# Kernel tuning notes

Hardware: AMD Instinct MI355X
Metric: run time of the kernel (lower is better)

The kernel has to match this reference:

```python
import jax, jax.numpy as jnp
import numpy as np

B, S, D = 2, 2048, 1024
H = 16
HD = D // H
MINUS_INFINITY = -1000000000.0


def setup_inputs() -> dict:
    key = jax.random.key(0)
    ks = jax.random.split(key, 6)
    sc = 0.02
    return {
        "x": jax.random.normal(ks[0], (B, S, D), dtype=jnp.float32),
        "Wq": jax.random.normal(ks[1], (D, D), dtype=jnp.float32) * sc,
        "Wk": jax.random.normal(ks[2], (D, D), dtype=jnp.float32) * sc,
        "Wv": jax.random.normal(ks[3], (D, D), dtype=jnp.float32) * sc,
        "Wo": jax.random.normal(ks[4], (D, D), dtype=jnp.float32) * sc,
        "bo": jnp.zeros((D,), dtype=jnp.float32),
    }


def reference(x, Wq, Wk, Wv, Wo, bo):
    b, n, _ = x.shape
    # Linear with transpose_b=True: x @ W.T
    q = jnp.einsum('bnd,ed->bne', x, Wq).reshape(b, n, H, HD).transpose(0, 2, 1, 3)
    k = jnp.einsum('bnd,ed->bne', x, Wk).reshape(b, n, H, HD).transpose(0, 2, 1, 3)
    v = jnp.einsum('bnd,ed->bne', x, Wv).reshape(b, n, H, HD).transpose(0, 2, 1, 3)
    scores = jnp.einsum('bhqd,bhkd->bhqk', q, k) * (1.0 / HD ** 0.5)
    mask = jnp.triu(jnp.ones((n, n), dtype=scores.dtype), k=1) * MINUS_INFINITY
    scores = scores + mask[None, None, :, :]
    attn = jax.nn.softmax(scores, axis=-1)  # dropout prob = 0.0
    ctx = jnp.einsum('bhqk,bhkd->bhqd', attn, v)
    ctx = ctx.transpose(0, 2, 1, 3).reshape(b, n, D)
    return jnp.einsum('bnd,ed->bne', ctx, Wo) + bo
```

## Files before the change

kernel.cpp:

```cpp
#include <hip/hip_runtime.h>
#include <hip/hip_bf16.h>

#define B_  2
#define S_  2048
#define D_  1024
#define H_  16
#define HD_ 64

typedef __attribute__((ext_vector_type(8))) short short8;
typedef __attribute__((ext_vector_type(4))) float f32x4;

__device__ __forceinline__ unsigned short f2b(float f) {
    __hip_bfloat16 h = __float2bfloat16(f);
    unsigned short u;
    __builtin_memcpy(&u, &h, 2);
    return u;
}

__device__ __forceinline__ float exp2_raw(float x) {
    float r;
    asm("v_exp_f32 %0, %1" : "=v"(r) : "v"(x));
    return r;
}

__device__ __forceinline__ unsigned int cvt_pk_bf16(float lo, float hi) {
    unsigned int r;
    asm("v_cvt_pk_bf16_f32 %0, %1, %2" : "=v"(r) : "v"(lo), "v"(hi));
    return r;
}

typedef __attribute__((address_space(1))) const unsigned int g_u32;
typedef __attribute__((address_space(3))) unsigned int l_u32;
__device__ __forceinline__ void gload_lds16(const void* g, void* l) {
    __builtin_amdgcn_global_load_lds((g_u32*)g, (l_u32*)l, 16, 0, 0);
}

__global__ __launch_bounds__(256) void convert_kernel(
    const float* __restrict__ x,  const float* __restrict__ Wq,
    const float* __restrict__ Wk, const float* __restrict__ Wv,
    const float* __restrict__ Wo, unsigned short* __restrict__ dst)
{
    const long long i4 = blockIdx.x * 256 + threadIdx.x;
    const long long e  = i4 * 4;
    const long long M1 = 1048576LL;
    const float* src;
    if      (e < 4 * M1) src = x  + e;
    else if (e < 5 * M1) src = Wq + (e - 4 * M1);
    else if (e < 6 * M1) src = Wk + (e - 5 * M1);
    else if (e < 7 * M1) src = Wv + (e - 6 * M1);
    else                 src = Wo + (e - 7 * M1);
    float4 v = *(const float4*)src;
    unsigned long long pk = (unsigned long long)f2b(v.x)
                          | ((unsigned long long)f2b(v.y) << 16)
                          | ((unsigned long long)f2b(v.z) << 32)
                          | ((unsigned long long)f2b(v.w) << 48);
    *(unsigned long long*)&dst[e] = pk;
}

__global__ __launch_bounds__(256) void qkv_proj_kernel(
    const unsigned short* __restrict__ x,
    const unsigned short* __restrict__ Wq,
    const unsigned short* __restrict__ Wk,
    const unsigned short* __restrict__ Wv,
    unsigned short* __restrict__ q_ws,
    unsigned short* __restrict__ k_ws,
    unsigned short* __restrict__ vT_ws)
{
    __shared__ unsigned short a_lds[128 * 64];
    __shared__ unsigned short b_lds[128 * 64];

    const int m0 = blockIdx.x * 128;
    const int n0 = blockIdx.y * 128;
    const int which = blockIdx.z;
    const unsigned short* W = (which == 0) ? Wq : (which == 1) ? Wk : Wv;

    const int tid  = threadIdx.x;
    const int wave = tid >> 6;
    const int lane = tid & 63;
    const int l15  = lane & 15;
    const int quad = lane >> 4;
    const int wm = (wave & 1) * 64;
    const int wn = (wave >> 1) * 64;
    const int xr = (l15 & 7) << 3;

    f32x4 acc[4][4];
    #pragma unroll
    for (int sm = 0; sm < 4; ++sm)
        #pragma unroll
        for (int sn = 0; sn < 4; ++sn)
            #pragma unroll
            for (int r = 0; r < 4; ++r) acc[sm][sn][r] = 0.f;

    for (int kk = 0; kk < D_; kk += 64) {
        #pragma unroll
        for (int p = 0; p < 4; ++p) {
            const int off = (p * 256 + tid) * 16;
            const int r   = off >> 7;
            const int cs  = ((off & 127) >> 1) ^ ((r & 7) << 3);
            gload_lds16(&x[(m0 + r) * D_ + kk + cs], &a_lds[off >> 1]);
            gload_lds16(&W[(n0 + r) * D_ + kk + cs], &b_lds[off >> 1]);
        }
        __syncthreads();
        #pragma unroll
        for (int kc = 0; kc < 2; ++kc) {
            const int cswz = (kc * 32 + quad * 8) ^ xr;
            short8 af[4], bf[4];
            #pragma unroll
            for (int s = 0; s < 4; ++s) {
                af[s] = *(const short8*)&a_lds[(wm + s * 16 + l15) * 64 + cswz];
                bf[s] = *(const short8*)&b_lds[(wn + s * 16 + l15) * 64 + cswz];
            }
            #pragma unroll
            for (int sm = 0; sm < 4; ++sm)
                #pragma unroll
                for (int sn = 0; sn < 4; ++sn)
                    acc[sm][sn] = __builtin_amdgcn_mfma_f32_16x16x32_bf16(
                        af[sm], bf[sn], acc[sm][sn], 0, 0, 0);
        }
        __syncthreads();
    }

    #pragma unroll
    for (int sm = 0; sm < 4; ++sm) {
        #pragma unroll
        for (int sn = 0; sn < 4; ++sn) {
            const int n  = n0 + wn + sn * 16 + l15;
            const int h  = n >> 6;
            const int hd = n & 63;
            const int mbase = m0 + wm + sm * 16 + quad * 4;
            const int b     = mbase >> 11;
            const int sbase = mbase & 2047;
            if (which == 2) {
                unsigned long long pk =
                      (unsigned long long)cvt_pk_bf16(acc[sm][sn][0], acc[sm][sn][1])
                    | ((unsigned long long)cvt_pk_bf16(acc[sm][sn][2], acc[sm][sn][3]) << 32);
                *(unsigned long long*)&vT_ws[((b * H_ + h) * HD_ + hd) * S_ + sbase] = pk;
            } else if (which == 0) {
                #pragma unroll
                for (int r = 0; r < 4; ++r)
                    q_ws[((b * H_ + h) * S_ + (sbase + r)) * HD_ + hd] =
                        f2b(acc[sm][sn][r] * (0.125f * 1.44269504f));
            } else {
                #pragma unroll
                for (int r = 0; r < 4; ++r)
                    k_ws[((b * H_ + h) * S_ + (sbase + r)) * HD_ + hd] =
                        f2b(acc[sm][sn][r]);
            }
        }
    }
}

__global__ __launch_bounds__(256) void attn_kernel(
    const unsigned short* __restrict__ q_ws,
    const unsigned short* __restrict__ k_ws,
    const unsigned short* __restrict__ vT_ws,
    unsigned short* __restrict__ ctx_ws)
{
    __shared__ unsigned short k_lds[2 * 64 * 64];
    __shared__ unsigned short vT_lds[2 * 64 * 64];

    const int bh = blockIdx.x;
    const int qt = 31 - (int)blockIdx.y;

    const int tid  = threadIdx.x;
    const int wave = tid >> 6;
    const int lane = tid & 63;
    const int l15  = lane & 15;
    const int quad = lane >> 4;
    const int r0   = tid >> 3;
    const int c8   = tid & 7;

    const unsigned short* Qh = q_ws + bh * (S_ * HD_);
    const unsigned short* Kh = k_ws + bh * (S_ * HD_);
    const unsigned short* Vt = vT_ws + bh * (HD_ * S_);
    const int b = bh >> 4;
    const int h = bh & 15;

    const int src0 = l15 + 32 * (quad & 1);
    const int src1 = src0 + 16;
    const int sel  = quad >> 1;

    const int qg = qt * 64 + wave * 16 + l15;

    const int scol = (c8 ^ (r0 & 7)) * 8;
    const int d0 = r0 * 64 + c8 * 8;
    const int d1 = d0 + 2048;
    const int xr8 = (l15 & 7) << 3;

    gload_lds16(&Kh[r0 * HD_ + scol],        &k_lds[d0]);
    gload_lds16(&Kh[(r0 + 32) * HD_ + scol], &k_lds[d1]);
    gload_lds16(&Vt[r0 * S_ + scol],         &vT_lds[d0]);
    gload_lds16(&Vt[(r0 + 32) * S_ + scol],  &vT_lds[d1]);

    short8 aq[2];
    aq[0] = *(const short8*)&Qh[qg * HD_ + quad * 8];
    aq[1] = *(const short8*)&Qh[qg * HD_ + 32 + quad * 8];

    __syncthreads();

    float l_lane = 0.f;
    f32x4 o[4];
    #pragma unroll
    for (int f = 0; f < 4; ++f)
        #pragma unroll
        for (int r = 0; r < 4; ++r) o[f][r] = 0.f;

    for (int kt = 0; kt <= qt; ++kt) {
        const int cb = (kt & 1) * 4096;
        if (kt < qt) {
            const int nk0 = (kt + 1) * 64;
            const int nbb = 4096 - cb;
            gload_lds16(&Kh[(nk0 + r0) * HD_ + scol],      &k_lds[nbb + d0]);
            gload_lds16(&Kh[(nk0 + r0 + 32) * HD_ + scol], &k_lds[nbb + d1]);
            gload_lds16(&Vt[r0 * S_ + nk0 + scol],         &vT_lds[nbb + d0]);
            gload_lds16(&Vt[(r0 + 32) * S_ + nk0 + scol],  &vT_lds[nbb + d1]);
        }

        f32x4 sc[4];
        #pragma unroll
        for (int f = 0; f < 4; ++f)
            #pragma unroll
            for (int r = 0; r < 4; ++r) sc[f][r] = 0.f;
        #pragma unroll
        for (int f = 0; f < 4; ++f)
            #pragma unroll
            for (int kc = 0; kc < 2; ++kc) {
                short8 ak = *(const short8*)&k_lds[cb + (f * 16 + l15) * 64
                                                  + ((kc * 32 + quad * 8) ^ xr8)];
                sc[f] = __builtin_amdgcn_mfma_f32_16x16x32_bf16(ak, aq[kc], sc[f], 0, 0, 0);
            }

        float p[4][4];
        if (kt == qt) {
            const int kbase = kt * 64 + quad * 4;
            #pragma unroll
            for (int f = 0; f < 4; ++f)
                #pragma unroll
                for (int r = 0; r < 4; ++r) {
                    const float pv = exp2_raw(sc[f][r]);
                    p[f][r] = (kbase + f * 16 + r > qg) ? 0.f : pv;
                    l_lane += p[f][r];
                }
        } else {
            #pragma unroll
            for (int f = 0; f < 4; ++f)
                #pragma unroll
                for (int r = 0; r < 4; ++r) {
                    p[f][r] = exp2_raw(sc[f][r]);
                    l_lane += p[f][r];
                }
        }

        unsigned int pd[4][2];
        #pragma unroll
        for (int f = 0; f < 4; ++f) {
            pd[f][0] = cvt_pk_bf16(p[f][0], p[f][1]);
            pd[f][1] = cvt_pk_bf16(p[f][2], p[f][3]);
        }

        #pragma unroll
        for (int c = 0; c < 2; ++c) {
            const int a0 = __shfl((int)pd[c * 2][0],     src0, 64);
            const int a1 = __shfl((int)pd[c * 2][1],     src0, 64);
            const int a2 = __shfl((int)pd[c * 2][0],     src1, 64);
            const int a3 = __shfl((int)pd[c * 2][1],     src1, 64);
            const int b0 = __shfl((int)pd[c * 2 + 1][0], src0, 64);
            const int b1 = __shfl((int)pd[c * 2 + 1][1], src0, 64);
            const int b2 = __shfl((int)pd[c * 2 + 1][0], src1, 64);
            const int b3 = __shfl((int)pd[c * 2 + 1][1], src1, 64);
            union { int i[4]; short8 s; } u2;
            u2.i[0] = sel ? b0 : a0;
            u2.i[1] = sel ? b1 : a1;
            u2.i[2] = sel ? b2 : a2;
            u2.i[3] = sel ? b3 : a3;
            #pragma unroll
            for (int f = 0; f < 4; ++f) {
                short8 av = *(const short8*)&vT_lds[cb + (f * 16 + l15) * 64
                                                   + ((c * 32 + quad * 8) ^ xr8)];
                o[f] = __builtin_amdgcn_mfma_f32_16x16x32_bf16(av, u2.s, o[f], 0, 0, 0);
            }
        }

        __syncthreads();
    }

    float l = l_lane;
    l += __shfl_xor(l, 16, 64);
    l += __shfl_xor(l, 32, 64);
    const float inv_l = 1.0f / l;

    #pragma unroll
    for (int f = 0; f < 4; ++f) {
        unsigned long long pk =
              (unsigned long long)cvt_pk_bf16(o[f][0] * inv_l, o[f][1] * inv_l)
            | ((unsigned long long)cvt_pk_bf16(o[f][2] * inv_l, o[f][3] * inv_l) << 32);
        *(unsigned long long*)&ctx_ws[(b * S_ + qg) * D_ + h * 64 + f * 16 + quad * 4] = pk;
    }
}

__global__ __launch_bounds__(256) void out_proj_kernel(
    const unsigned short* __restrict__ ctx,
    const unsigned short* __restrict__ Wo,
    const float* __restrict__ bo,
    float* __restrict__ out)
{
    __shared__ unsigned short a_lds[128 * 64];
    __shared__ unsigned short b_lds[128 * 64];

    const int m0 = blockIdx.x * 128;
    const int n0 = blockIdx.y * 128;

    const int tid  = threadIdx.x;
    const int wave = tid >> 6;
    const int lane = tid & 63;
    const int l15  = lane & 15;
    const int quad = lane >> 4;
    const int wm = (wave & 1) * 64;
    const int wn = (wave >> 1) * 64;
    const int xr = (l15 & 7) << 3;

    f32x4 acc[4][4];
    #pragma unroll
    for (int sm = 0; sm < 4; ++sm)
        #pragma unroll
        for (int sn = 0; sn < 4; ++sn)
            #pragma unroll
            for (int r = 0; r < 4; ++r) acc[sm][sn][r] = 0.f;

    for (int kk = 0; kk < D_; kk += 64) {
        #pragma unroll
        for (int p = 0; p < 4; ++p) {
            const int off = (p * 256 + tid) * 16;
            const int r   = off >> 7;
            const int cs  = ((off & 127) >> 1) ^ ((r & 7) << 3);
            gload_lds16(&ctx[(m0 + r) * D_ + kk + cs], &a_lds[off >> 1]);
            gload_lds16(&Wo[(n0 + r) * D_ + kk + cs],  &b_lds[off >> 1]);
        }
        __syncthreads();
        #pragma unroll
        for (int kc = 0; kc < 2; ++kc) {
            const int cswz = (kc * 32 + quad * 8) ^ xr;
            short8 af[4], bf[4];
            #pragma unroll
            for (int s = 0; s < 4; ++s) {
                af[s] = *(const short8*)&a_lds[(wm + s * 16 + l15) * 64 + cswz];
                bf[s] = *(const short8*)&b_lds[(wn + s * 16 + l15) * 64 + cswz];
            }
            #pragma unroll
            for (int sm = 0; sm < 4; ++sm)
                #pragma unroll
                for (int sn = 0; sn < 4; ++sn)
                    acc[sm][sn] = __builtin_amdgcn_mfma_f32_16x16x32_bf16(
                        af[sm], bf[sn], acc[sm][sn], 0, 0, 0);
        }
        __syncthreads();
    }

    #pragma unroll
    for (int sm = 0; sm < 4; ++sm) {
        #pragma unroll
        for (int sn = 0; sn < 4; ++sn) {
            const int n = n0 + wn + sn * 16 + l15;
            const float bias = bo[n];
            const int mbase = m0 + wm + sm * 16 + quad * 4;
            #pragma unroll
            for (int r = 0; r < 4; ++r)
                out[(mbase + r) * D_ + n] = acc[sm][sn][r] + bias;
        }
    }
}

extern "C" void kernel_launch(void* const* d_in, const int* in_sizes, int n_in,
                              void* d_out, int out_size, void* d_ws, size_t ws_size,
                              hipStream_t stream) {
    const float* x  = (const float*)d_in[0];
    const float* Wq = (const float*)d_in[1];
    const float* Wk = (const float*)d_in[2];
    const float* Wv = (const float*)d_in[3];
    const float* Wo = (const float*)d_in[4];
    const float* bo = (const float*)d_in[5];
    float* out = (float*)d_out;

    const size_t M1 = 1048576;
    const size_t SZ = 4 * M1;

    unsigned short* xb  = (unsigned short*)d_ws;
    unsigned short* wqb = xb  + SZ;
    unsigned short* wkb = wqb + M1;
    unsigned short* wvb = wkb + M1;
    unsigned short* wob = wvb + M1;
    unsigned short* q_ws   = wob + M1;
    unsigned short* k_ws   = q_ws + SZ;
    unsigned short* vT_ws  = k_ws + SZ;
    unsigned short* ctx_ws = vT_ws + SZ;

    convert_kernel<<<dim3(8192), 256, 0, stream>>>(x, Wq, Wk, Wv, Wo, xb);
    qkv_proj_kernel<<<dim3(32, 8, 3), 256, 0, stream>>>(xb, wqb, wkb, wvb, q_ws, k_ws, vT_ws);
    attn_kernel<<<dim3(32, 32), 256, 0, stream>>>(q_ws, k_ws, vT_ws, ctx_ws);
    out_proj_kernel<<<dim3(32, 8), 256, 0, stream>>>(ctx_ws, wob, bo, out);
}
```

Measured before the change: 192.3 us.

## Double-buffer LDS tiles in projection GEMMs with K=32 prefetch

Restructures the QKV and output projection GEMM main loops to use two LDS buffers of K=32 tiles. The next tile is loaded asynchronously while MFMAs run on the current one. The goal is to hide global-to-LDS latency that the single-buffered loop exposed. The XOR swizzle is removed and barriers per K are doubled, which may introduce LDS bank conflicts and sync overhead.

```diff
diff --git a/kernel.cpp b/kernel.cpp
--- a/kernel.cpp
+++ b/kernel.cpp
@@ -66,8 +66,8 @@
     unsigned short* __restrict__ k_ws,
     unsigned short* __restrict__ vT_ws)
 {
-    __shared__ unsigned short a_lds[128 * 64];
-    __shared__ unsigned short b_lds[128 * 64];
+    __shared__ unsigned short a_lds[2][128 * 32];
+    __shared__ unsigned short b_lds[2][128 * 32];
 
     const int m0 = blockIdx.x * 128;
     const int n0 = blockIdx.y * 128;
@@ -81,7 +81,10 @@
     const int quad = lane >> 4;
     const int wm = (wave & 1) * 64;
     const int wn = (wave >> 1) * 64;
-    const int xr = (l15 & 7) << 3;
+
+    const int srow = tid >> 2;
+    const int scol = (tid & 3) * 8;
+    const int soff = tid * 8;
 
     f32x4 acc[4][4];
     #pragma unroll
@@ -91,32 +94,37 @@
             #pragma unroll
             for (int r = 0; r < 4; ++r) acc[sm][sn][r] = 0.f;
 
-    for (int kk = 0; kk < D_; kk += 64) {
-        #pragma unroll
-        for (int p = 0; p < 4; ++p) {
-            const int off = (p * 256 + tid) * 16;
-            const int r   = off >> 7;
-            const int cs  = ((off & 127) >> 1) ^ ((r & 7) << 3);
-            gload_lds16(&x[(m0 + r) * D_ + kk + cs], &a_lds[off >> 1]);
-            gload_lds16(&W[(n0 + r) * D_ + kk + cs], &b_lds[off >> 1]);
-        }
-        __syncthreads();
-        #pragma unroll
-        for (int kc = 0; kc < 2; ++kc) {
-            const int cswz = (kc * 32 + quad * 8) ^ xr;
-            short8 af[4], bf[4];
-            #pragma unroll
-            for (int s = 0; s < 4; ++s) {
-                af[s] = *(const short8*)&a_lds[(wm + s * 16 + l15) * 64 + cswz];
-                bf[s] = *(const short8*)&b_lds[(wn + s * 16 + l15) * 64 + cswz];
+    #pragma unroll
+    for (int p = 0; p < 2; ++p) {
+        gload_lds16(&x[(m0 + srow + p * 64) * D_ + scol], &a_lds[0][p * 2048 + soff]);
+        gload_lds16(&W[(n0 + srow + p * 64) * D_ + scol], &b_lds[0][p * 2048 + soff]);
+    }
+    __syncthreads();
+
+    for (int t = 0; t < 32; ++t) {
+        const int cur = t & 1;
+        if (t < 31) {
+            const int kk = (t + 1) * 32;
+            #pragma unroll
+            for (int p = 0; p < 2; ++p) {
+                gload_lds16(&x[(m0 + srow + p * 64) * D_ + kk + scol],
+                            &a_lds[cur ^ 1][p * 2048 + soff]);
+                gload_lds16(&W[(n0 + srow + p * 64) * D_ + kk + scol],
+                            &b_lds[cur ^ 1][p * 2048 + soff]);
             }
-            #pragma unroll
-            for (int sm = 0; sm < 4; ++sm)
-                #pragma unroll
-                for (int sn = 0; sn < 4; ++sn)
-                    acc[sm][sn] = __builtin_amdgcn_mfma_f32_16x16x32_bf16(
-                        af[sm], bf[sn], acc[sm][sn], 0, 0, 0);
-        }
+        }
+        short8 af[4], bf[4];
+        #pragma unroll
+        for (int s = 0; s < 4; ++s) {
+            af[s] = *(const short8*)&a_lds[cur][(wm + s * 16 + l15) * 32 + quad * 8];
+            bf[s] = *(const short8*)&b_lds[cur][(wn + s * 16 + l15) * 32 + quad * 8];
+        }
+        #pragma unroll
+        for (int sm = 0; sm < 4; ++sm)
+            #pragma unroll
+            for (int sn = 0; sn < 4; ++sn)
+                acc[sm][sn] = __builtin_amdgcn_mfma_f32_16x16x32_bf16(
+                    af[sm], bf[sn], acc[sm][sn], 0, 0, 0);
         __syncthreads();
     }
 
@@ -304,8 +312,8 @@
     const float* __restrict__ bo,
     float* __restrict__ out)
 {
-    __shared__ unsigned short a_lds[128 * 64];
-    __shared__ unsigned short b_lds[128 * 64];
+    __shared__ unsigned short a_lds[2][128 * 32];
+    __shared__ unsigned short b_lds[2][128 * 32];
 
     const int m0 = blockIdx.x * 128;
     const int n0 = blockIdx.y * 128;
@@ -317,7 +325,10 @@
     const int quad = lane >> 4;
     const int wm = (wave & 1) * 64;
     const int wn = (wave >> 1) * 64;
-    const int xr = (l15 & 7) << 3;
+
+    const int srow = tid >> 2;
+    const int scol = (tid & 3) * 8;
+    const int soff = tid * 8;
 
     f32x4 acc[4][4];
     #pragma unroll
@@ -327,32 +338,37 @@
             #pragma unroll
             for (int r = 0; r < 4; ++r) acc[sm][sn][r] = 0.f;
 
-    for (int kk = 0; kk < D_; kk += 64) {
-        #pragma unroll
-        for (int p = 0; p < 4; ++p) {
-            const int off = (p * 256 + tid) * 16;
-            const int r   = off >> 7;
-            const int cs  = ((off & 127) >> 1) ^ ((r & 7) << 3);
-            gload_lds16(&ctx[(m0 + r) * D_ + kk + cs], &a_lds[off >> 1]);
-            gload_lds16(&Wo[(n0 + r) * D_ + kk + cs],  &b_lds[off >> 1]);
-        }
-        __syncthreads();
-        #pragma unroll
-        for (int kc = 0; kc < 2; ++kc) {
-            const int cswz = (kc * 32 + quad * 8) ^ xr;
-            short8 af[4], bf[4];
-            #pragma unroll
-            for (int s = 0; s < 4; ++s) {
-                af[s] = *(const short8*)&a_lds[(wm + s * 16 + l15) * 64 + cswz];
-                bf[s] = *(const short8*)&b_lds[(wn + s * 16 + l15) * 64 + cswz];
+    #pragma unroll
+    for (int p = 0; p < 2; ++p) {
+        gload_lds16(&ctx[(m0 + srow + p * 64) * D_ + scol], &a_lds[0][p * 2048 + soff]);
+        gload_lds16(&Wo[(n0 + srow + p * 64) * D_ + scol],  &b_lds[0][p * 2048 + soff]);
+    }
+    __syncthreads();
+
+    for (int t = 0; t < 32; ++t) {
+        const int cur = t & 1;
+        if (t < 31) {
+            const int kk = (t + 1) * 32;
+            #pragma unroll
+            for (int p = 0; p < 2; ++p) {
+                gload_lds16(&ctx[(m0 + srow + p * 64) * D_ + kk + scol],
+                            &a_lds[cur ^ 1][p * 2048 + soff]);
+                gload_lds16(&Wo[(n0 + srow + p * 64) * D_ + kk + scol],
+                            &b_lds[cur ^ 1][p * 2048 + soff]);
             }
-            #pragma unroll
-            for (int sm = 0; sm < 4; ++sm)
-                #pragma unroll
-                for (int sn = 0; sn < 4; ++sn)
-                    acc[sm][sn] = __builtin_amdgcn_mfma_f32_16x16x32_bf16(
-                        af[sm], bf[sn], acc[sm][sn], 0, 0, 0);
-        }
+        }
+        short8 af[4], bf[4];
+        #pragma unroll
+        for (int s = 0; s < 4; ++s) {
+            af[s] = *(const short8*)&a_lds[cur][(wm + s * 16 + l15) * 32 + quad * 8];
+            bf[s] = *(const short8*)&b_lds[cur][(wn + s * 16 + l15) * 32 + quad * 8];
+        }
+        #pragma unroll
+        for (int sm = 0; sm < 4; ++sm)
+            #pragma unroll
+            for (int sn = 0; sn < 4; ++sn)
+                acc[sm][sn] = __builtin_amdgcn_mfma_f32_16x16x32_bf16(
+                    af[sm], bf[sn], acc[sm][sn], 0, 0, 0);
         __syncthreads();
     }
 
```

Result: no change. 191.6 us, median of 3 (-0.4%).
